# Optimization experiments

Hardware: AMD Instinct MI355X
Metric: run time of the kernel (lower is better)

## Reference

```python
import jax, jax.numpy as jnp
import numpy as np
from functools import partial

N = 512
H, W = 324, 332
C = 120
NEAR, FAR, BG = 0.01, 100.0, 1.0


def setup_inputs() -> dict:
    key = jax.random.key(0)
    k1, k2, k3, k4, k5, k6 = jax.random.split(key, 6)
    # positions: small xy, depth z in [2, 8] so everything projects on screen
    xy = 0.5 * jax.random.normal(k1, (N, 2), dtype=jnp.float32)
    z = jax.random.uniform(k2, (N, 1), dtype=jnp.float32, minval=2.0, maxval=8.0)
    positions = jnp.concatenate([xy, z], axis=-1)  # [N,3]
    rotations = jax.random.normal(k3, (N, 4), dtype=jnp.float32)  # unused by the math
    # scales in [0.5, 4.5] pixels -> small footprints, early-break never triggers
    scales = jax.random.uniform(k4, (N, 3), dtype=jnp.float32) * 4.0 + 0.5
    opacities = jax.random.uniform(k5, (N,), dtype=jnp.float32)
    spectral_features = jax.random.uniform(k6, (N, C), dtype=jnp.float32)
    tone_mapping = jnp.ones((C,), dtype=jnp.float32)
    intrinsics = jnp.array([[300.0, 0.0, 166.0],
                            [0.0, 300.0, 162.0],
                            [0.0, 0.0, 1.0]], dtype=jnp.float32)
    extrinsics = jnp.eye(4, dtype=jnp.float32)
    return {"positions": positions, "rotations": rotations, "scales": scales,
            "opacities": opacities, "spectral_features": spectral_features,
            "tone_mapping": tone_mapping, "intrinsics": intrinsics,
            "extrinsics": extrinsics}


def _render(positions, scales, opacities, spectral_features, tone_mapping,
            intrinsics, extrinsics):
    # --- projection (world -> camera -> screen) ---
    ph = jnp.concatenate([positions, jnp.ones_like(positions[:, :1])], axis=-1)  # [N,4]
    cam = ph @ extrinsics.T                     # [N,4]
    cam3 = cam[:, :3]
    proj = cam3 @ intrinsics.T                  # [N,3]
    screen = proj[:, :2] / (proj[:, 2:3] + 1e-6)  # [N,2] (x, y)
    depths = cam3[:, 2]                         # [N]

    # --- frustum / screen culling mask (kept as a validity flag) ---
    valid = (depths > NEAR) & (depths < FAR)
    valid &= (screen[:, 0] > -100.0) & (screen[:, 0] < W + 100.0)
    valid &= (screen[:, 1] > -100.0) & (screen[:, 1] < H + 100.0)

    # --- 2D covariance: diag(scale_x^2, scale_y^2), regularized inverse ---
    s2 = scales[:, :2] ** 2
    cov = jnp.zeros((positions.shape[0], 2, 2), dtype=positions.dtype)
    cov = cov.at[:, 0, 0].set(s2[:, 0]).at[:, 1, 1].set(s2[:, 1])
    cov_inv = jnp.linalg.inv(cov + 1e-4 * jnp.eye(2, dtype=positions.dtype))  # [N,2,2]

    # --- depth sort (front to back) ---
    order = jnp.argsort(depths)
    screen_s = screen[order]
    depths_s = depths[order]
    cinv_s = cov_inv[order]
    op_s = opacities[order]
    valid_s = valid[order]
    spec_s = spectral_features[order]           # [N,C]

    # pixel grid: pix[h,w] = (x=w, y=h)
    X, Y = jnp.meshgrid(jnp.arange(W), jnp.arange(H))  # each [H,W]
    pix = jnp.stack([X, Y], axis=-1).astype(positions.dtype)  # [H,W,2]

    def step(A, g):
        pos, cinv, op, v = g
        done = jnp.mean(A) > 0.99  # torch early-break condition
        off = (pos[0] < -W) | (pos[0] > 2 * W) | (pos[1] < -H) | (pos[1] > 2 * H)
        skip = done | off | jnp.logical_not(v)
        diff = pix - pos                                    # [H,W,2]
        mahal = jnp.einsum('hwi,ij,hwj->hw', diff, cinv, diff)
        alpha = op * jnp.exp(-0.5 * mahal) * (1.0 - A)      # [H,W]
        alpha = jnp.where(skip, 0.0, alpha)
        return A + alpha, alpha

    A0 = jnp.zeros((H, W), dtype=positions.dtype)
    A_final, alphas = jax.lax.scan(step, A0, (screen_s, cinv_s, op_s, valid_s))  # alphas [N,H,W]

    # spectral/depth accumulation == sum_i feature_i * alpha_i (GEMM over N)
    spectral = jnp.einsum('nc,nhw->chw', spec_s, alphas)    # [C,H,W]
    depth_img = jnp.einsum('n,nhw->hw', depths_s, alphas)   # [H,W]
    spectral = spectral + BG * (1.0 - A_final)[None]
    spectral = spectral * tone_mapping[:, None, None]
    return spectral, depth_img, A_final


def reference(positions, rotations, scales, opacities, spectral_features,
              tone_mapping, intrinsics, extrinsics):
    # rotations are accepted but unused by the original math (diagonal 2D cov)
    return _render(positions, scales, opacities, spectral_features,
                   tone_mapping, intrinsics, extrinsics)
```

## Files before the change

### kernel.cpp

```cpp
#include <hip/hip_runtime.h>
#include <math.h>

#define N_G 512
#define IMG_H 324
#define IMG_W 332
#define N_C 120
#define HW (IMG_H*IMG_W)
#define CHUNK 64
#define TSX 21
#define TSY 81
#define NT (TSX*TSY)
#define NBLK 512


__global__ __launch_bounds__(512) void k_prep(
    const float* __restrict__ pos, const float* __restrict__ scales,
    const float* __restrict__ opac, const float* __restrict__ K,
    const float* __restrict__ E,
    float4* __restrict__ bb, float* __restrict__ ps, int* __restrict__ cnt)
{
  __shared__ float key[N_G];
  const int i = threadIdx.x;
  if (i == 0) *cnt = 0;

  float p0 = pos[i*3+0], p1 = pos[i*3+1], p2 = pos[i*3+2];
  float cam0 = E[0]*p0 + E[1]*p1 + E[2]*p2  + E[3];
  float cam1 = E[4]*p0 + E[5]*p1 + E[6]*p2  + E[7];
  float cam2 = E[8]*p0 + E[9]*p1 + E[10]*p2 + E[11];
  float pr0 = K[0]*cam0 + K[1]*cam1 + K[2]*cam2;
  float pr1 = K[3]*cam0 + K[4]*cam1 + K[5]*cam2;
  float pr2 = K[6]*cam0 + K[7]*cam1 + K[8]*cam2;
  float inv = 1.0f/(pr2 + 1e-6f);
  float sx = pr0*inv, sy = pr1*inv;
  float depth = cam2;

  bool valid = (depth > 0.01f) && (depth < 100.0f)
            && (sx > -100.0f) && (sx < (float)IMG_W + 100.0f)
            && (sy > -100.0f) && (sy < (float)IMG_H + 100.0f);
  bool off = (sx < -(float)IMG_W) || (sx > 2.0f*(float)IMG_W)
          || (sy < -(float)IMG_H) || (sy > 2.0f*(float)IMG_H);
  bool skip = off || (!valid);

  float s0 = scales[i*3+0], s1 = scales[i*3+1];
  float v0 = s0*s0 + 1e-4f, v1 = s1*s1 + 1e-4f;
  const float HL2E = 0.72134752f;
  float c00s = HL2E/v0, c11s = HL2E/v1;
  float op = skip ? 0.0f : opac[i];
  float l2op = __log2f(op);
  float rx = 6.0f*sqrtf(v0);
  float ry = 6.0f*sqrtf(v1);
  float xmin = skip ?  1e9f : sx - rx;
  float xmax = skip ? -1e9f : sx + rx;
  float ymin = skip ?  1e9f : sy - ry;
  float ymax = skip ? -1e9f : sy + ry;

  key[i] = depth;
  __syncthreads();

  int rank = 0;
  #pragma unroll 4
  for (int j = 0; j < N_G; j += 4) {
    float4 k4 = *(const float4*)&key[j];
    rank += (k4.x < depth || (k4.x == depth && j+0 < i)) ? 1 : 0;
    rank += (k4.y < depth || (k4.y == depth && j+1 < i)) ? 1 : 0;
    rank += (k4.z < depth || (k4.z == depth && j+2 < i)) ? 1 : 0;
    rank += (k4.w < depth || (k4.w == depth && j+3 < i)) ? 1 : 0;
  }

  bb[rank] = make_float4(xmin, xmax, ymin, ymax);
  *(float4*)&ps[rank*8]   = make_float4(sx, sy, c00s, c11s);
  *(float4*)&ps[rank*8+4] = make_float4(l2op, depth, __int_as_float(i*N_C), 0.0f);
}

#define ACC4(i) \
  { float4 s4 = *(const float4*)(row + 4*(i)); \
    a##i.x = fmaf(wv, s4.x, a##i.x); \
    a##i.y = fmaf(wv, s4.y, a##i.y); \
    a##i.z = fmaf(wv, s4.z, a##i.z); \
    a##i.w = fmaf(wv, s4.w, a##i.w); }

#define WR4(i) \
  { slot[4*(i)+0]=a##i.x; slot[4*(i)+1]=a##i.y; \
    slot[4*(i)+2]=a##i.z; slot[4*(i)+3]=a##i.w; }

#define CMB4(i) \
  { float4 t4 = *(const float4*)(tmh + 4*(i)); \
    out[(cbase + 4*(i) + 0)*HW + pixi] = (a##i.x + slot[4*(i)+0] + bgT)*t4.x; \
    out[(cbase + 4*(i) + 1)*HW + pixi] = (a##i.y + slot[4*(i)+1] + bgT)*t4.y; \
    out[(cbase + 4*(i) + 2)*HW + pixi] = (a##i.z + slot[4*(i)+2] + bgT)*t4.z; \
    out[(cbase + 4*(i) + 3)*HW + pixi] = (a##i.w + slot[4*(i)+3] + bgT)*t4.w; }

__global__ __launch_bounds__(256, 2) void k_render(
    const float4* __restrict__ bb, const float* __restrict__ ps,
    int* __restrict__ cnt, const float* __restrict__ spec,
    const float* __restrict__ tm, float* __restrict__ out)
{
  __shared__ float prm[N_G*8];
  __shared__ float buf[CHUNK*64];
  __shared__ float sbuf[CHUNK*N_C];
  __shared__ float Tcar[64], Dcar[64];
  __shared__ int wcnt[4];
  __shared__ int stile;

  const int tid  = threadIdx.x;
  const int w    = tid >> 6;
  const int lane = tid & 63;
  const int h    = w & 1;
  const int s    = w >> 1;
  const int tx = lane & 15, ty = lane >> 4;
  const int cbase = h*60;
  const unsigned long long ltm = (1ull << lane) - 1ull;

  for (;;) {
    if (tid == 0) stile = atomicAdd(cnt, 1);
    __syncthreads();
    const int t = stile;
    if (t >= NT) break;
    const int jx = t % TSX, ky = t / TSX;
    const int bx = 10 + ((jx & 1) ? ((jx+1)>>1) : -((jx+1)>>1));
    const int by = 40 + ((ky & 1) ? ((ky+1)>>1) : -((ky+1)>>1));

    const int x = bx*16 + tx;
    const int y = by*4 + ty;
    const bool inb = (x < IMG_W) && (y < IMG_H);
    const float px = (float)min(x, IMG_W-1);
    const float py = (float)min(y, IMG_H-1);
    const float wxmin = (float)(bx*16), wxmax = wxmin + 15.0f;
    const float wymin = (float)(by*4),  wymax = wymin + 3.0f;

    const int g0 = w*128 + lane;
    const int g1 = g0 + 64;
    float4 b0 = bb[g0], b1 = bb[g1];
    bool h0 = !(b0.x > wxmax || b0.y < wxmin || b0.z > wymax || b0.w < wymin);
    bool h1 = !(b1.x > wxmax || b1.y < wxmin || b1.z > wymax || b1.w < wymin);
    unsigned long long m0 = __ballot(h0), m1 = __ballot(h1);
    int c0 = __popcll(m0), c1 = __popcll(m1);
    if (lane == 0) wcnt[w] = c0 + c1;
    __syncthreads();
    int offw = 0;
    #pragma unroll
    for (int k = 0; k < 4; ++k) if (k < w) offw += wcnt[k];
    const int nh = wcnt[0] + wcnt[1] + wcnt[2] + wcnt[3];
    if (h0) {
      int p = offw + __popcll(m0 & ltm);
      *(float4*)&prm[p*8]   = *(const float4*)&ps[g0*8];
      *(float4*)&prm[p*8+4] = *(const float4*)&ps[g0*8+4];
    }
    if (h1) {
      int p = offw + c0 + __popcll(m1 & ltm);
      *(float4*)&prm[p*8]   = *(const float4*)&ps[g1*8];
      *(float4*)&prm[p*8+4] = *(const float4*)&ps[g1*8+4];
    }
    __syncthreads();

    float T = 1.0f, dacc = 0.0f;
    float4 a0={0,0,0,0}, a1={0,0,0,0}, a2={0,0,0,0}, a3={0,0,0,0}, a4={0,0,0,0},
           a5={0,0,0,0}, a6={0,0,0,0}, a7={0,0,0,0}, a8={0,0,0,0}, a9={0,0,0,0},
           a10={0,0,0,0}, a11={0,0,0,0}, a12={0,0,0,0}, a13={0,0,0,0}, a14={0,0,0,0};

    for (int cb = 0; cb < nh; cb += CHUNK) {
      const int nc = min(CHUNK, nh - cb);

      #pragma unroll 2
      for (int j = w; j < nc; j += 4) {
        float4 p0 = *(const float4*)&prm[(cb+j)*8];
        float4 p1 = *(const float4*)&prm[(cb+j)*8+4];
        float dx = px - p0.x, dy = py - p0.y;
        float m = p0.z*dx*dx + p0.w*dy*dy;
        buf[j*64 + lane] = exp2f(p1.x - m);
        int sbase = __float_as_int(p1.z);
        sbuf[j*N_C + lane] = spec[sbase + lane];
        if (lane < N_C - 64) sbuf[j*N_C + 64 + lane] = spec[sbase + 64 + lane];
      }
      __syncthreads();

      if (w == 0) {
        #pragma unroll 4
        for (int j = 0; j < nc; ++j) {
          float a = buf[j*64 + lane];
          float wv = a * T;
          buf[j*64 + lane] = wv;
          T -= wv;
          dacc = fmaf(prm[(cb+j)*8+5], wv, dacc);
        }
      }
      __syncthreads();

      #pragma unroll 2
      for (int j = s; j < nc; j += 2) {
        float wv = buf[j*64 + lane];
        const float* row = &sbuf[j*N_C + cbase];
        ACC4(0)  ACC4(1)  ACC4(2)  ACC4(3)  ACC4(4)
        ACC4(5)  ACC4(6)  ACC4(7)  ACC4(8)  ACC4(9)
        ACC4(10) ACC4(11) ACC4(12) ACC4(13) ACC4(14)
      }
      __syncthreads();
    }

    if (w == 0) { Tcar[lane] = T; Dcar[lane] = dacc; }
    if (s == 1) {
      float* slot = (h == 0 ? buf : sbuf) + lane*61;
      WR4(0)  WR4(1)  WR4(2)  WR4(3)  WR4(4)
      WR4(5)  WR4(6)  WR4(7)  WR4(8)  WR4(9)
      WR4(10) WR4(11) WR4(12) WR4(13) WR4(14)
    }
    __syncthreads();

    if (s == 0 && inb) {
      const int pixi = y*IMG_W + x;
      const float Tf = Tcar[lane];
      const float bgT = Tf;
      const float* tmh = tm + cbase;
      const float* slot = (h == 0 ? buf : sbuf) + lane*61;
      CMB4(0)  CMB4(1)  CMB4(2)  CMB4(3)  CMB4(4)
      CMB4(5)  CMB4(6)  CMB4(7)  CMB4(8)  CMB4(9)
      CMB4(10) CMB4(11) CMB4(12) CMB4(13) CMB4(14)
      if (h == 0) out[N_C*HW + pixi] = Dcar[lane];
      else        out[N_C*HW + HW + pixi] = 1.0f - Tf;
    }
    __syncthreads();
  }
}

extern "C" void kernel_launch(void* const* d_in, const int* in_sizes, int n_in,
                              void* d_out, int out_size, void* d_ws, size_t ws_size,
                              hipStream_t stream) {
  const float* pos    = (const float*)d_in[0];
  const float* scales = (const float*)d_in[2];
  const float* opac   = (const float*)d_in[3];
  const float* spec   = (const float*)d_in[4];
  const float* tm     = (const float*)d_in[5];
  const float* K      = (const float*)d_in[6];
  const float* E      = (const float*)d_in[7];
  float* out = (float*)d_out;

  float4* bb = (float4*)d_ws;
  float*  ps = (float*)(bb + N_G);
  int*    cnt = (int*)((char*)d_ws + N_G*16 + N_G*32);

  k_prep<<<1, 512, 0, stream>>>(pos, scales, opac, K, E, bb, ps, cnt);
  k_render<<<NBLK, 256, 0, stream>>>(bb, ps, cnt, spec, tm, out);
}
```

Measured before the change: 127.8 us.

## Fuse projection and depth sort into render kernel with per-tile sorting

Removes the separate single-block prep kernel. Each render block now projects the gaussians itself and keeps their parameters in registers, then depth-sorts only the gaussians that hit the tile by rank counting in shared memory. The atomic work queue is replaced by a static grid-stride tile loop. This saves a kernel launch and the serial dependency between the two kernels, at the cost of doing the projection redundantly in every block, adding a per-tile sort, and losing dynamic load balancing.

```diff
diff --git a/kernel.cpp b/kernel.cpp
--- a/kernel.cpp
+++ b/kernel.cpp
@@ -13,65 +13,6 @@
 #define NBLK 512
 
 
-__global__ __launch_bounds__(512) void k_prep(
-    const float* __restrict__ pos, const float* __restrict__ scales,
-    const float* __restrict__ opac, const float* __restrict__ K,
-    const float* __restrict__ E,
-    float4* __restrict__ bb, float* __restrict__ ps, int* __restrict__ cnt)
-{
-  __shared__ float key[N_G];
-  const int i = threadIdx.x;
-  if (i == 0) *cnt = 0;
-
-  float p0 = pos[i*3+0], p1 = pos[i*3+1], p2 = pos[i*3+2];
-  float cam0 = E[0]*p0 + E[1]*p1 + E[2]*p2  + E[3];
-  float cam1 = E[4]*p0 + E[5]*p1 + E[6]*p2  + E[7];
-  float cam2 = E[8]*p0 + E[9]*p1 + E[10]*p2 + E[11];
-  float pr0 = K[0]*cam0 + K[1]*cam1 + K[2]*cam2;
-  float pr1 = K[3]*cam0 + K[4]*cam1 + K[5]*cam2;
-  float pr2 = K[6]*cam0 + K[7]*cam1 + K[8]*cam2;
-  float inv = 1.0f/(pr2 + 1e-6f);
-  float sx = pr0*inv, sy = pr1*inv;
-  float depth = cam2;
-
-  bool valid = (depth > 0.01f) && (depth < 100.0f)
-            && (sx > -100.0f) && (sx < (float)IMG_W + 100.0f)
-            && (sy > -100.0f) && (sy < (float)IMG_H + 100.0f);
-  bool off = (sx < -(float)IMG_W) || (sx > 2.0f*(float)IMG_W)
-          || (sy < -(float)IMG_H) || (sy > 2.0f*(float)IMG_H);
-  bool skip = off || (!valid);
-
-  float s0 = scales[i*3+0], s1 = scales[i*3+1];
-  float v0 = s0*s0 + 1e-4f, v1 = s1*s1 + 1e-4f;
-  const float HL2E = 0.72134752f;
-  float c00s = HL2E/v0, c11s = HL2E/v1;
-  float op = skip ? 0.0f : opac[i];
-  float l2op = __log2f(op);
-  float rx = 6.0f*sqrtf(v0);
-  float ry = 6.0f*sqrtf(v1);
-  float xmin = skip ?  1e9f : sx - rx;
-  float xmax = skip ? -1e9f : sx + rx;
-  float ymin = skip ?  1e9f : sy - ry;
-  float ymax = skip ? -1e9f : sy + ry;
-
-  key[i] = depth;
-  __syncthreads();
-
-  int rank = 0;
-  #pragma unroll 4
-  for (int j = 0; j < N_G; j += 4) {
-    float4 k4 = *(const float4*)&key[j];
-    rank += (k4.x < depth || (k4.x == depth && j+0 < i)) ? 1 : 0;
-    rank += (k4.y < depth || (k4.y == depth && j+1 < i)) ? 1 : 0;
-    rank += (k4.z < depth || (k4.z == depth && j+2 < i)) ? 1 : 0;
-    rank += (k4.w < depth || (k4.w == depth && j+3 < i)) ? 1 : 0;
-  }
-
-  bb[rank] = make_float4(xmin, xmax, ymin, ymax);
-  *(float4*)&ps[rank*8]   = make_float4(sx, sy, c00s, c11s);
-  *(float4*)&ps[rank*8+4] = make_float4(l2op, depth, __int_as_float(i*N_C), 0.0f);
-}
-
 #define ACC4(i) \
   { float4 s4 = *(const float4*)(row + 4*(i)); \
     a##i.x = fmaf(wv, s4.x, a##i.x); \
@@ -91,8 +32,9 @@
     out[(cbase + 4*(i) + 3)*HW + pixi] = (a##i.w + slot[4*(i)+3] + bgT)*t4.w; }
 
 __global__ __launch_bounds__(256, 2) void k_render(
-    const float4* __restrict__ bb, const float* __restrict__ ps,
-    int* __restrict__ cnt, const float* __restrict__ spec,
+    const float* __restrict__ pos, const float* __restrict__ scales,
+    const float* __restrict__ opac, const float* __restrict__ Km,
+    const float* __restrict__ Em, const float* __restrict__ spec,
     const float* __restrict__ tm, float* __restrict__ out)
 {
   __shared__ float prm[N_G*8];
@@ -100,7 +42,6 @@
   __shared__ float sbuf[CHUNK*N_C];
   __shared__ float Tcar[64], Dcar[64];
   __shared__ int wcnt[4];
-  __shared__ int stile;
 
   const int tid  = threadIdx.x;
   const int w    = tid >> 6;
@@ -111,11 +52,51 @@
   const int cbase = h*60;
   const unsigned long long ltm = (1ull << lane) - 1ull;
 
-  for (;;) {
-    if (tid == 0) stile = atomicAdd(cnt, 1);
-    __syncthreads();
-    const int t = stile;
-    if (t >= NT) break;
+  float psx[2], psy[2], pc00[2], pc11[2], pl2[2], pd[2];
+  float bxmin[2], bxmax[2], bymin[2], bymax[2];
+  {
+    const float E0=Em[0],E1=Em[1],E2=Em[2],E3=Em[3],
+                E4=Em[4],E5=Em[5],E6=Em[6],E7=Em[7],
+                E8=Em[8],E9=Em[9],E10=Em[10],E11=Em[11];
+    const float K0=Km[0],K1=Km[1],K2=Km[2],
+                K3=Km[3],K4=Km[4],K5=Km[5],
+                K6=Km[6],K7=Km[7],K8=Km[8];
+    #pragma unroll
+    for (int q = 0; q < 2; ++q) {
+      const int g = w*128 + lane + q*64;
+      float p0 = pos[g*3+0], p1 = pos[g*3+1], p2 = pos[g*3+2];
+      float cam0 = E0*p0 + E1*p1 + E2*p2  + E3;
+      float cam1 = E4*p0 + E5*p1 + E6*p2  + E7;
+      float cam2 = E8*p0 + E9*p1 + E10*p2 + E11;
+      float pr0 = K0*cam0 + K1*cam1 + K2*cam2;
+      float pr1 = K3*cam0 + K4*cam1 + K5*cam2;
+      float pr2 = K6*cam0 + K7*cam1 + K8*cam2;
+      float inv = 1.0f/(pr2 + 1e-6f);
+      float sx = pr0*inv, sy = pr1*inv;
+      float depth = cam2;
+      bool valid = (depth > 0.01f) && (depth < 100.0f)
+                && (sx > -100.0f) && (sx < (float)IMG_W + 100.0f)
+                && (sy > -100.0f) && (sy < (float)IMG_H + 100.0f);
+      bool off = (sx < -(float)IMG_W) || (sx > 2.0f*(float)IMG_W)
+              || (sy < -(float)IMG_H) || (sy > 2.0f*(float)IMG_H);
+      bool skip = off || (!valid);
+      float s0 = scales[g*3+0], s1 = scales[g*3+1];
+      float v0 = s0*s0 + 1e-4f, v1 = s1*s1 + 1e-4f;
+      const float HL2E = 0.72134752f;
+      psx[q] = sx; psy[q] = sy;
+      pc00[q] = HL2E/v0; pc11[q] = HL2E/v1;
+      pl2[q] = __log2f(skip ? 0.0f : opac[g]);
+      pd[q]  = depth;
+      float rx = 6.0f*sqrtf(v0);
+      float ry = 6.0f*sqrtf(v1);
+      bxmin[q] = skip ?  1e9f : sx - rx;
+      bxmax[q] = skip ? -1e9f : sx + rx;
+      bymin[q] = skip ?  1e9f : sy - ry;
+      bymax[q] = skip ? -1e9f : sy + ry;
+    }
+  }
+
+  for (int t = blockIdx.x; t < NT; t += NBLK) {
     const int jx = t % TSX, ky = t / TSX;
     const int bx = 10 + ((jx & 1) ? ((jx+1)>>1) : -((jx+1)>>1));
     const int by = 40 + ((ky & 1) ? ((ky+1)>>1) : -((ky+1)>>1));
@@ -128,28 +109,53 @@
     const float wxmin = (float)(bx*16), wxmax = wxmin + 15.0f;
     const float wymin = (float)(by*4),  wymax = wymin + 3.0f;
 
-    const int g0 = w*128 + lane;
-    const int g1 = g0 + 64;
-    float4 b0 = bb[g0], b1 = bb[g1];
-    bool h0 = !(b0.x > wxmax || b0.y < wxmin || b0.z > wymax || b0.w < wymin);
-    bool h1 = !(b1.x > wxmax || b1.y < wxmin || b1.z > wymax || b1.w < wymin);
+    bool h0 = !(bxmin[0] > wxmax || bxmax[0] < wxmin ||
+                bymin[0] > wymax || bymax[0] < wymin);
+    bool h1 = !(bxmin[1] > wxmax || bxmax[1] < wxmin ||
+                bymin[1] > wymax || bymax[1] < wymin);
     unsigned long long m0 = __ballot(h0), m1 = __ballot(h1);
-    int c0 = __popcll(m0), c1 = __popcll(m1);
-    if (lane == 0) wcnt[w] = c0 + c1;
+    int c0 = __popcll(m0);
+    if (lane == 0) wcnt[w] = c0 + __popcll(m1);
     __syncthreads();
     int offw = 0;
     #pragma unroll
     for (int k = 0; k < 4; ++k) if (k < w) offw += wcnt[k];
     const int nh = wcnt[0] + wcnt[1] + wcnt[2] + wcnt[3];
-    if (h0) {
-      int p = offw + __popcll(m0 & ltm);
-      *(float4*)&prm[p*8]   = *(const float4*)&ps[g0*8];
-      *(float4*)&prm[p*8+4] = *(const float4*)&ps[g0*8+4];
-    }
-    if (h1) {
-      int p = offw + c0 + __popcll(m1 & ltm);
-      *(float4*)&prm[p*8]   = *(const float4*)&ps[g1*8];
-      *(float4*)&prm[p*8+4] = *(const float4*)&ps[g1*8+4];
+    const int p0 = offw + __popcll(m0 & ltm);
+    const int p1 = offw + c0 + __popcll(m1 & ltm);
+    if (h0) buf[p0] = pd[0];
+    if (h1) buf[p1] = pd[1];
+    if (tid < 4) buf[nh + tid] = 1e30f;
+    __syncthreads();
+
+    if (h0 | h1) {
+      int r0 = 0, r1 = 0;
+      const float d0 = pd[0], d1 = pd[1];
+      for (int j = 0; j < nh; j += 4) {
+        float4 k4 = *(const float4*)&buf[j];
+        if (h0) {
+          r0 += (k4.x < d0 || (k4.x == d0 && j+0 < p0)) ? 1 : 0;
+          r0 += (k4.y < d0 || (k4.y == d0 && j+1 < p0)) ? 1 : 0;
+          r0 += (k4.z < d0 || (k4.z == d0 && j+2 < p0)) ? 1 : 0;
+          r0 += (k4.w < d0 || (k4.w == d0 && j+3 < p0)) ? 1 : 0;
+        }
+        if (h1) {
+          r1 += (k4.x < d1 || (k4.x == d1 && j+0 < p1)) ? 1 : 0;
+          r1 += (k4.y < d1 || (k4.y == d1 && j+1 < p1)) ? 1 : 0;
+          r1 += (k4.z < d1 || (k4.z == d1 && j+2 < p1)) ? 1 : 0;
+          r1 += (k4.w < d1 || (k4.w == d1 && j+3 < p1)) ? 1 : 0;
+        }
+      }
+      if (h0) {
+        *(float4*)&prm[r0*8]   = make_float4(psx[0], psy[0], pc00[0], pc11[0]);
+        *(float4*)&prm[r0*8+4] = make_float4(pl2[0], pd[0],
+                                   __int_as_float((w*128 + lane)*N_C), 0.0f);
+      }
+      if (h1) {
+        *(float4*)&prm[r1*8]   = make_float4(psx[1], psy[1], pc00[1], pc11[1]);
+        *(float4*)&prm[r1*8+4] = make_float4(pl2[1], pd[1],
+                                   __int_as_float((w*128 + lane + 64)*N_C), 0.0f);
+      }
     }
     __syncthreads();
 
@@ -163,12 +169,12 @@
 
       #pragma unroll 2
       for (int j = w; j < nc; j += 4) {
-        float4 p0 = *(const float4*)&prm[(cb+j)*8];
-        float4 p1 = *(const float4*)&prm[(cb+j)*8+4];
-        float dx = px - p0.x, dy = py - p0.y;
-        float m = p0.z*dx*dx + p0.w*dy*dy;
-        buf[j*64 + lane] = exp2f(p1.x - m);
-        int sbase = __float_as_int(p1.z);
+        float4 q0 = *(const float4*)&prm[(cb+j)*8];
+        float4 q1 = *(const float4*)&prm[(cb+j)*8+4];
+        float dx = px - q0.x, dy = py - q0.y;
+        float m = q0.z*dx*dx + q0.w*dy*dy;
+        buf[j*64 + lane] = exp2f(q1.x - m);
+        int sbase = __float_as_int(q1.z);
         sbuf[j*N_C + lane] = spec[sbase + lane];
         if (lane < N_C - 64) sbuf[j*N_C + 64 + lane] = spec[sbase + 64 + lane];
       }
@@ -233,11 +239,7 @@
   const float* K      = (const float*)d_in[6];
   const float* E      = (const float*)d_in[7];
   float* out = (float*)d_out;
-
-  float4* bb = (float4*)d_ws;
-  float*  ps = (float*)(bb + N_G);
-  int*    cnt = (int*)((char*)d_ws + N_G*16 + N_G*32);
-
-  k_prep<<<1, 512, 0, stream>>>(pos, scales, opac, K, E, bb, ps, cnt);
-  k_render<<<NBLK, 256, 0, stream>>>(bb, ps, cnt, spec, tm, out);
+  (void)d_ws; (void)ws_size;
+
+  k_render<<<NBLK, 256, 0, stream>>>(pos, scales, opac, K, E, spec, tm, out);
 }
```

Measured after the change: 124.0 us. -3.0%, faster.
